# Kernel tuning notes

Measured on AMD Instinct MI355X. Metric: run time of the kernel, lower is better.

Reference implementation:

```python
import jax, jax.numpy as jnp
import numpy as np

N0, N1, N2 = 200000, 100000, 50000
E0, E1 = 1600000, 800000
D_IN, H, C, K = 256, 256, 7, 40  # in_feats, n_hidden, center_num, n_classes


def setup_inputs() -> dict:
    key = jax.random.key(0)
    ks = jax.random.split(key, 11)
    s = 0.05
    inputs = jax.random.normal(ks[0], (N0, D_IN), jnp.float32)
    edge_src0 = jax.random.randint(ks[1], (E0,), 0, N0, jnp.int32)
    edge_dst0 = jax.random.randint(ks[2], (E0,), 0, N1, jnp.int32)
    edge_src1 = jax.random.randint(ks[3], (E1,), 0, N1, jnp.int32)
    edge_dst1 = jax.random.randint(ks[4], (E1,), 0, N2, jnp.int32)
    W_self0 = jax.random.normal(ks[5], (H, D_IN), jnp.float32) * s
    W_neigh0 = jax.random.normal(ks[6], (H, D_IN), jnp.float32) * s
    b0 = jnp.zeros((H,), jnp.float32)
    W_self1 = jax.random.normal(ks[7], (H, H), jnp.float32) * s
    W_neigh1 = jax.random.normal(ks[8], (H, H), jnp.float32) * s
    b1 = jnp.zeros((H,), jnp.float32)
    W_prompt = jax.random.normal(ks[9], (C, 2 * H), jnp.float32) * s
    W_pp = jax.random.normal(ks[10], (C, K, 2 * H), jnp.float32) * s
    return dict(inputs=inputs, W_self0=W_self0, W_neigh0=W_neigh0, b0=b0,
                W_self1=W_self1, W_neigh1=W_neigh1, b1=b1,
                W_prompt=W_prompt, W_pp=W_pp,
                edge_src0=edge_src0, edge_dst0=edge_dst0,
                edge_src1=edge_src1, edge_dst1=edge_dst1)


def _sage_conv(h_src, h_dst, esrc, edst, n_dst, W_self, W_neigh, b):
    # DGL SAGEConv('mean'): fc_self(h_dst) + fc_neigh(mean_{u in N(v)} h_src[u]) + bias
    msg = h_src[esrc]                                            # [E, d]
    summ = jax.ops.segment_sum(msg, edst, num_segments=n_dst)    # [n_dst, d]
    deg = jax.ops.segment_sum(jnp.ones((esrc.shape[0],), msg.dtype), edst,
                              num_segments=n_dst)                # [n_dst]
    mean = summ / jnp.maximum(deg, 1.0)[:, None]
    return h_dst @ W_self.T + mean @ W_neigh.T + b


def _forward(inputs, W_self0, W_neigh0, b0, W_self1, W_neigh1, b1,
             W_prompt, W_pp, edge_src0, edge_dst0, edge_src1, edge_dst1):
    h = inputs  # dropout=0.0 (eval): identity
    # layer 0: N0 src -> N1 dst
    h_dst = h[:N1]
    h = _sage_conv(h, h_dst, edge_src0, edge_dst0, N1, W_self0, W_neigh0, b0)
    h = jax.nn.relu(h)
    # layer 1: N1 src -> N2 dst
    h_dst = h[:N2]
    h = _sage_conv(h, h_dst, edge_src1, edge_dst1, N2, W_self1, W_neigh1, b1)
    h = jax.nn.relu(h)
    neighbor = jax.nn.relu(h_dst)
    hcat = jnp.concatenate([h, neighbor], axis=1)                # [N2, 2H]
    scores = hcat @ W_prompt.T                                   # [N2, C]
    index = jnp.argmax(scores, axis=1)                           # [N2]
    # per-cluster expert Linear, top-1 dispatch/combine
    all_out = jnp.einsum('nd,ckd->nck', hcat, W_pp)              # [N2, C, K]
    out = jnp.take_along_axis(all_out, index[:, None, None], axis=1)[:, 0, :]
    return out


def reference(inputs, W_self0, W_neigh0, b0, W_self1, W_neigh1, b1,
              W_prompt, W_pp, edge_src0, edge_dst0, edge_src1, edge_dst1):
    return _forward(inputs, W_self0, W_neigh0, b0, W_self1, W_neigh1, b1,
                    W_prompt, W_pp, edge_src0, edge_dst0, edge_src1, edge_dst1)
```

## Files before the change

kernel.cpp:

```cpp
#include <hip/hip_runtime.h>
#include <stdint.h>

typedef unsigned short u16;
typedef unsigned int   u32;
typedef float f32x4  __attribute__((ext_vector_type(4)));
typedef _Float16 f16x4 __attribute__((ext_vector_type(4)));
typedef _Float16 f16x8 __attribute__((ext_vector_type(8)));

#define NN0 200000
#define NN1 100000
#define NN2 50000
#define EE0 1600000
#define EE1 800000
#define DD  256
#define CC  7
#define KK  40
#define NHEAD 288

#define LVL2_U16 4096
#define IMG_U16  8192

static __device__ __forceinline__ void split2(float x, _Float16& t0, _Float16& t1) {
    t0 = (_Float16)x;
    t1 = (_Float16)(x - (float)t0);
}

static __device__ __forceinline__ f16x8 pack8(const _Float16* h) {
    f16x8 v;
#pragma unroll
    for (int i = 0; i < 8; ++i) v[i] = h[i];
    return v;
}

static __device__ __forceinline__ void async16(const void* g, void* l) {
    __builtin_amdgcn_global_load_lds(
        (const __attribute__((address_space(1))) void*)g,
        (__attribute__((address_space(3))) void*)l, 16, 0, 0);
}

__global__ void hist_kernel(const int* __restrict__ dst, int* __restrict__ cnt, int n) {
    int i = blockIdx.x * blockDim.x + threadIdx.x;
    if (i < n) atomicAdd(&cnt[dst[i]], 1);
}

__global__ void scan_block_kernel(const int* __restrict__ in, int* __restrict__ out,
                                  int* __restrict__ partials, int n) {
    __shared__ int sd[256];
    int t = threadIdx.x;
    int base = blockIdx.x * 1024 + t * 4;
    int v0 = (base + 0 < n) ? in[base + 0] : 0;
    int v1 = (base + 1 < n) ? in[base + 1] : 0;
    int v2 = (base + 2 < n) ? in[base + 2] : 0;
    int v3 = (base + 3 < n) ? in[base + 3] : 0;
    int p0 = v0, p1 = p0 + v1, p2 = p1 + v2, p3 = p2 + v3;
    sd[t] = p3;
    __syncthreads();
    for (int off = 1; off < 256; off <<= 1) {
        int x = (t >= off) ? sd[t - off] : 0;
        __syncthreads();
        sd[t] += x;
        __syncthreads();
    }
    int excl = sd[t] - p3;
    if (base + 0 < n) out[base + 0] = excl + p0;
    if (base + 1 < n) out[base + 1] = excl + p1;
    if (base + 2 < n) out[base + 2] = excl + p2;
    if (base + 3 < n) out[base + 3] = excl + p3;
    if (t == 255) partials[blockIdx.x] = sd[255];
}

__global__ void scan_partials_kernel(int* __restrict__ partials, int nb) {
    __shared__ int sd[256];
    int t = threadIdx.x;
    int v = (t < nb) ? partials[t] : 0;
    sd[t] = v;
    __syncthreads();
    for (int off = 1; off < 256; off <<= 1) {
        int x = (t >= off) ? sd[t - off] : 0;
        __syncthreads();
        sd[t] += x;
        __syncthreads();
    }
    if (t < nb) partials[t] = sd[t];
}

__global__ void scan_add_kernel(int* __restrict__ out, const int* __restrict__ partials, int n) {
    int b = blockIdx.x;
    if (b == 0) return;
    int add = partials[b - 1];
    int base = b * 1024 + threadIdx.x * 4;
    if (base + 0 < n) out[base + 0] += add;
    if (base + 1 < n) out[base + 1] += add;
    if (base + 2 < n) out[base + 2] += add;
    if (base + 3 < n) out[base + 3] += add;
}

__global__ void fill_kernel(const int* __restrict__ esrc, const int* __restrict__ edst,
                            const int* __restrict__ rp, int* __restrict__ cur,
                            int* __restrict__ ss, int n) {
    int i = blockIdx.x * blockDim.x + threadIdx.x;
    if (i < n) {
        int d = edst[i];
        int p = rp[d] + atomicAdd(&cur[d], 1);
        ss[p] = esrc[i];
    }
}

__global__ void to_fp16(const float* __restrict__ in, _Float16* __restrict__ outp, long n) {
    long i = ((long)blockIdx.x * blockDim.x + threadIdx.x) * 8;
    if (i >= n) return;
    f32x4 a = *reinterpret_cast<const f32x4*>(in + i);
    f32x4 b = *reinterpret_cast<const f32x4*>(in + i + 4);
    f16x8 h;
    h[0] = (_Float16)a[0]; h[1] = (_Float16)a[1]; h[2] = (_Float16)a[2]; h[3] = (_Float16)a[3];
    h[4] = (_Float16)b[0]; h[5] = (_Float16)b[1]; h[6] = (_Float16)b[2]; h[7] = (_Float16)b[3];
    *reinterpret_cast<f16x8*>(outp + i) = h;
}

__global__ void gather_mean_fp16(const _Float16* __restrict__ Xh, const int* __restrict__ rp,
                                 const int* __restrict__ ss, float* __restrict__ mean, int ndst) {
    int wave = threadIdx.x >> 6, lane = threadIdx.x & 63;
    int d = blockIdx.x * 4 + wave;
    if (d >= ndst) return;
    int beg = rp[d], end = rp[d + 1];
    int lo4 = lane * 4;
    f32x4 a0 = (f32x4)(0.f), a1 = (f32x4)(0.f), a2 = (f32x4)(0.f), a3 = (f32x4)(0.f);
    int j = beg;
    for (; j + 8 <= end; j += 8) {
        int s0 = ss[j + 0], s1 = ss[j + 1], s2 = ss[j + 2], s3 = ss[j + 3];
        int s4 = ss[j + 4], s5 = ss[j + 5], s6 = ss[j + 6], s7 = ss[j + 7];
        f16x4 h0 = *reinterpret_cast<const f16x4*>(Xh + (size_t)s0 * DD + lo4);
        f16x4 h1 = *reinterpret_cast<const f16x4*>(Xh + (size_t)s1 * DD + lo4);
        f16x4 h2 = *reinterpret_cast<const f16x4*>(Xh + (size_t)s2 * DD + lo4);
        f16x4 h3 = *reinterpret_cast<const f16x4*>(Xh + (size_t)s3 * DD + lo4);
        f16x4 h4 = *reinterpret_cast<const f16x4*>(Xh + (size_t)s4 * DD + lo4);
        f16x4 h5 = *reinterpret_cast<const f16x4*>(Xh + (size_t)s5 * DD + lo4);
        f16x4 h6 = *reinterpret_cast<const f16x4*>(Xh + (size_t)s6 * DD + lo4);
        f16x4 h7 = *reinterpret_cast<const f16x4*>(Xh + (size_t)s7 * DD + lo4);
        a0 += __builtin_convertvector(h0, f32x4);
        a1 += __builtin_convertvector(h1, f32x4);
        a2 += __builtin_convertvector(h2, f32x4);
        a3 += __builtin_convertvector(h3, f32x4);
        a0 += __builtin_convertvector(h4, f32x4);
        a1 += __builtin_convertvector(h5, f32x4);
        a2 += __builtin_convertvector(h6, f32x4);
        a3 += __builtin_convertvector(h7, f32x4);
    }
    for (; j + 4 <= end; j += 4) {
        int s0 = ss[j + 0], s1 = ss[j + 1], s2 = ss[j + 2], s3 = ss[j + 3];
        f16x4 h0 = *reinterpret_cast<const f16x4*>(Xh + (size_t)s0 * DD + lo4);
        f16x4 h1 = *reinterpret_cast<const f16x4*>(Xh + (size_t)s1 * DD + lo4);
        f16x4 h2 = *reinterpret_cast<const f16x4*>(Xh + (size_t)s2 * DD + lo4);
        f16x4 h3 = *reinterpret_cast<const f16x4*>(Xh + (size_t)s3 * DD + lo4);
        a0 += __builtin_convertvector(h0, f32x4);
        a1 += __builtin_convertvector(h1, f32x4);
        a2 += __builtin_convertvector(h2, f32x4);
        a3 += __builtin_convertvector(h3, f32x4);
    }
    for (; j < end; ++j) {
        int s = ss[j];
        f16x4 h0 = *reinterpret_cast<const f16x4*>(Xh + (size_t)s * DD + lo4);
        a0 += __builtin_convertvector(h0, f32x4);
    }
    f32x4 s = (a0 + a1) + (a2 + a3);
    int dg = end - beg;
    float inv = 1.0f / (float)(dg > 0 ? dg : 1);
    s *= inv;
    *reinterpret_cast<f32x4*>(mean + (size_t)d * DD + lo4) = s;
}

__global__ void build_wimg(const float* __restrict__ Wa0, const float* __restrict__ Wb0,
                           const float* __restrict__ Wa1, const float* __restrict__ Wb1,
                           u16* __restrict__ img) {
    int blk = blockIdx.x;
    int layer = blk >> 5;
    int ntile = (blk >> 4) & 1;
    int chunk = blk & 15;
    const float* Wa = layer ? Wa1 : Wa0;
    const float* Wb = layer ? Wb1 : Wb0;
    int t = threadIdx.x;
    int row = t >> 1, half = t & 1;
    int n = ntile * 128 + row;
    int kg = chunk * 32 + half * 16;
    const float* W = (kg < 256) ? Wa : Wb;
    int kk = kg & 255;
    const float* src = W + (size_t)n * 256 + kk;
    float x[16];
#pragma unroll
    for (int j = 0; j < 16; j += 4) {
        float4 v = *reinterpret_cast<const float4*>(src + j);
        x[j] = v.x; x[j + 1] = v.y; x[j + 2] = v.z; x[j + 3] = v.w;
    }
    _Float16 h0[16], h1[16];
#pragma unroll
    for (int j = 0; j < 16; ++j) split2(x[j], h0[j], h1[j]);
    int rs = (row >> 1) & 3;
    int q0 = (half * 2 + 0) ^ rs;
    int q1 = (half * 2 + 1) ^ rs;
    u16* base = img + (size_t)blk * IMG_U16 + row * 32;
    *reinterpret_cast<f16x8*>(base + q0 * 8)            = pack8(h0);
    *reinterpret_cast<f16x8*>(base + q1 * 8)            = pack8(h0 + 8);
    *reinterpret_cast<f16x8*>(base + LVL2_U16 + q0 * 8) = pack8(h1);
    *reinterpret_cast<f16x8*>(base + LVL2_U16 + q1 * 8) = pack8(h1 + 8);
}

__global__ void build_wimg_head(const float* __restrict__ Wp, const float* __restrict__ Wpp,
                                u16* __restrict__ img) {
    int blk = blockIdx.x;
    int ntile = blk >> 4;
    int chunk = blk & 15;
    int t = threadIdx.x;
    int row = t >> 1, half = t & 1;
    int r = ntile * 128 + row;
    int kg = chunk * 32 + half * 16;
    float x[16];
    const float* src = nullptr;
    if (r < CC)            src = Wp  + (size_t)r * 512 + kg;
    else if (r < CC + CC * KK) src = Wpp + (size_t)(r - CC) * 512 + kg;
    if (src) {
#pragma unroll
        for (int j = 0; j < 16; j += 4) {
            float4 v = *reinterpret_cast<const float4*>(src + j);
            x[j] = v.x; x[j + 1] = v.y; x[j + 2] = v.z; x[j + 3] = v.w;
        }
    } else {
#pragma unroll
        for (int j = 0; j < 16; ++j) x[j] = 0.f;
    }
    _Float16 h0[16], h1[16];
#pragma unroll
    for (int j = 0; j < 16; ++j) split2(x[j], h0[j], h1[j]);
    int rs = (row >> 1) & 3;
    int q0 = (half * 2 + 0) ^ rs;
    int q1 = (half * 2 + 1) ^ rs;
    u16* base = img + (size_t)blk * IMG_U16 + row * 32;
    *reinterpret_cast<f16x8*>(base + q0 * 8)            = pack8(h0);
    *reinterpret_cast<f16x8*>(base + q1 * 8)            = pack8(h0 + 8);
    *reinterpret_cast<f16x8*>(base + LVL2_U16 + q0 * 8) = pack8(h1);
    *reinterpret_cast<f16x8*>(base + LVL2_U16 + q1 * 8) = pack8(h1 + 8);
}

__global__ __launch_bounds__(256, 3) void gemm_f16(const float* __restrict__ X0,
                                                   const float* __restrict__ X1,
                                                   const u16* __restrict__ imgL,
                                                   const float* __restrict__ bias,
                                                   float* __restrict__ out,
                                                   _Float16* __restrict__ outh,
                                                   int M, int ldo, int dorelu) {
    __shared__ __align__(16) u16 Asl[2 * LVL2_U16];
    __shared__ __align__(16) u16 Bsl[2 * LVL2_U16];
    int t = threadIdx.x;
    int wave = t >> 6, lane = t & 63;
    int m0 = blockIdx.x * 128;
    int ntile = blockIdx.y;
    int wy = wave >> 1, wx = wave & 1;

    f32x4 acc[4][4];
#pragma unroll
    for (int i = 0; i < 4; ++i)
#pragma unroll
        for (int j = 0; j < 4; ++j) acc[i][j] = (f32x4)(0.f);

    int arow_l = t >> 1;
    int akh = t & 1;
    int arow = m0 + arow_l; if (arow >= M) arow = M - 1;

    int fr = lane & 15;
    int q  = lane >> 4;
    int frm = wy * 64 + fr;
    int frn = wx * 64 + fr;

    const u16* imgT = imgL + (size_t)ntile * 16 * IMG_U16;

    for (int c = 0; c < 16; ++c) {
        const char* src = (const char*)(imgT + (size_t)c * IMG_U16);
#pragma unroll
        for (int i = 0; i < 4; ++i) {
            int seg = wave * 4 + i;
            async16(src + seg * 1024 + lane * 16, (char*)Bsl + seg * 1024 + lane * 16);
        }
        {
            const float* Xs = (c < 8) ? X0 : X1;
            int kc = (c & 7) * 32;
            const float* p = Xs + (size_t)arow * 256 + kc + akh * 16;
            float x[16];
#pragma unroll
            for (int j = 0; j < 16; j += 4) {
                float4 v = *reinterpret_cast<const float4*>(p + j);
                x[j] = v.x; x[j + 1] = v.y; x[j + 2] = v.z; x[j + 3] = v.w;
            }
            _Float16 h0[16], h1[16];
#pragma unroll
            for (int j = 0; j < 16; ++j) split2(x[j], h0[j], h1[j]);
            int rs = (arow_l >> 1) & 3;
            int q0 = (akh * 2 + 0) ^ rs;
            int q1 = (akh * 2 + 1) ^ rs;
            u16* d = Asl + arow_l * 32;
            *reinterpret_cast<f16x8*>(d + q0 * 8)            = pack8(h0);
            *reinterpret_cast<f16x8*>(d + q1 * 8)            = pack8(h0 + 8);
            *reinterpret_cast<f16x8*>(d + LVL2_U16 + q0 * 8) = pack8(h1);
            *reinterpret_cast<f16x8*>(d + LVL2_U16 + q1 * 8) = pack8(h1 + 8);
        }
        __syncthreads();
        f16x8 bf[4][2];
#pragma unroll
        for (int ns = 0; ns < 4; ++ns) {
            int r = frn + ns * 16;
            int off = r * 32 + ((q ^ ((r >> 1) & 3))) * 8;
            bf[ns][0] = *reinterpret_cast<const f16x8*>(Bsl + off);
            bf[ns][1] = *reinterpret_cast<const f16x8*>(Bsl + LVL2_U16 + off);
        }
#pragma unroll
        for (int ms = 0; ms < 4; ++ms) {
            int r = frm + ms * 16;
            int off = r * 32 + ((q ^ ((r >> 1) & 3))) * 8;
            f16x8 af0 = *reinterpret_cast<const f16x8*>(Asl + off);
            f16x8 af1 = *reinterpret_cast<const f16x8*>(Asl + LVL2_U16 + off);
#pragma unroll
            for (int ns = 0; ns < 4; ++ns) {
                f32x4 a = acc[ms][ns];
                a = __builtin_amdgcn_mfma_f32_16x16x32_f16(af0, bf[ns][0], a, 0, 0, 0);
                a = __builtin_amdgcn_mfma_f32_16x16x32_f16(af0, bf[ns][1], a, 0, 0, 0);
                a = __builtin_amdgcn_mfma_f32_16x16x32_f16(af1, bf[ns][0], a, 0, 0, 0);
                acc[ms][ns] = a;
            }
        }
        __syncthreads();
    }
#pragma unroll
    for (int ms = 0; ms < 4; ++ms) {
        int rbase = m0 + wy * 64 + ms * 16 + (lane >> 4) * 4;
#pragma unroll
        for (int ns = 0; ns < 4; ++ns) {
            int col = ntile * 128 + wx * 64 + ns * 16 + (lane & 15);
            if (col >= ldo) continue;
            float bcol = bias ? bias[col] : 0.f;
#pragma unroll
            for (int r = 0; r < 4; ++r) {
                int row = rbase + r;
                if (row < M) {
                    float v = acc[ms][ns][r] + bcol;
                    if (dorelu) v = fmaxf(v, 0.f);
                    out[(size_t)row * ldo + col] = v;
                    if (outh) outh[(size_t)row * DD + col] = (_Float16)v;
                }
            }
        }
    }
}

__global__ void select_kernel(const float* __restrict__ all, float* __restrict__ out) {
    int wave = threadIdx.x >> 6, lane = threadIdx.x & 63;
    int n = blockIdx.x * 4 + wave;
    if (n >= NN2) return;
    const float* row = all + (size_t)n * NHEAD;
    float best = row[0]; int bc = 0;
#pragma unroll
    for (int c = 1; c < CC; ++c) {
        float s = row[c];
        if (s > best) { best = s; bc = c; }
    }
    if (lane < KK) out[(size_t)n * KK + lane] = row[CC + bc * KK + lane];
}

extern "C" void kernel_launch(void* const* d_in, const int* in_sizes, int n_in,
                              void* d_out, int out_size, void* d_ws, size_t ws_size,
                              hipStream_t stream) {
    const float* inputs  = (const float*)d_in[0];
    const float* Wself0  = (const float*)d_in[1];
    const float* Wneigh0 = (const float*)d_in[2];
    const float* b0      = (const float*)d_in[3];
    const float* Wself1  = (const float*)d_in[4];
    const float* Wneigh1 = (const float*)d_in[5];
    const float* b1      = (const float*)d_in[6];
    const float* Wp      = (const float*)d_in[7];
    const float* Wpp     = (const float*)d_in[8];
    const int* es0 = (const int*)d_in[9];
    const int* ed0 = (const int*)d_in[10];
    const int* es1 = (const int*)d_in[11];
    const int* ed1 = (const int*)d_in[12];

    char* ws = (char*)d_ws;
    size_t off = 0;
    auto alloc = [&](size_t bytes) -> void* {
        void* p = (void*)(ws + off);
        off += (bytes + 255) & ~(size_t)255;
        return p;
    };
    int* cnt0 = (int*)alloc((size_t)NN1 * 4);
    int* cnt1 = (int*)alloc((size_t)NN2 * 4);
    int* cur0 = (int*)alloc((size_t)NN1 * 4);
    int* cur1 = (int*)alloc((size_t)NN2 * 4);
    int* rp0  = (int*)alloc((size_t)(NN1 + 1) * 4);
    int* rp1  = (int*)alloc((size_t)(NN2 + 1) * 4);
    int* part0 = (int*)alloc(1024);
    int* part1 = (int*)alloc(1024);
    size_t zero_bytes = off;
    int*   ss0   = (int*)alloc((size_t)EE0 * 4);
    int*   ss1   = (int*)alloc((size_t)EE1 * 4);
    u16*   wimg  = (u16*)alloc((size_t)(64 + 48) * IMG_U16 * 2);
    u16*   wimgH = wimg + (size_t)64 * IMG_U16;
    _Float16* xh = (_Float16*)alloc((size_t)NN0 * DD * 2);
    float*    h1 = (float*)xh;
    _Float16* h1h  = (_Float16*)alloc((size_t)NN1 * DD * 2);
    float* mean0 = (float*)alloc((size_t)NN1 * DD * 4);
    float* mean1 = mean0;
    float* h2    = mean0 + (size_t)NN2 * DD;
    float* allout = (float*)alloc((size_t)NN2 * NHEAD * 4);

    hipMemsetAsync(d_ws, 0, zero_bytes, stream);

    hist_kernel<<<(EE0 + 255) / 256, 256, 0, stream>>>(ed0, cnt0, EE0);
    hist_kernel<<<(EE1 + 255) / 256, 256, 0, stream>>>(ed1, cnt1, EE1);
    int nb0 = (NN1 + 1023) / 1024, nb1 = (NN2 + 1023) / 1024;
    scan_block_kernel<<<nb0, 256, 0, stream>>>(cnt0, rp0 + 1, part0, NN1);
    scan_partials_kernel<<<1, 256, 0, stream>>>(part0, nb0);
    scan_add_kernel<<<nb0, 256, 0, stream>>>(rp0 + 1, part0, NN1);
    scan_block_kernel<<<nb1, 256, 0, stream>>>(cnt1, rp1 + 1, part1, NN2);
    scan_partials_kernel<<<1, 256, 0, stream>>>(part1, nb1);
    scan_add_kernel<<<nb1, 256, 0, stream>>>(rp1 + 1, part1, NN2);
    fill_kernel<<<(EE0 + 255) / 256, 256, 0, stream>>>(es0, ed0, rp0, cur0, ss0, EE0);
    fill_kernel<<<(EE1 + 255) / 256, 256, 0, stream>>>(es1, ed1, rp1, cur1, ss1, EE1);

    build_wimg<<<64, 256, 0, stream>>>(Wself0, Wneigh0, Wself1, Wneigh1, wimg);
    build_wimg_head<<<48, 256, 0, stream>>>(Wp, Wpp, wimgH);

    long nx = (long)NN0 * DD;
    to_fp16<<<(int)(nx / 8 / 256), 256, 0, stream>>>(inputs, xh, nx);

    gather_mean_fp16<<<(NN1 + 3) / 4, 256, 0, stream>>>(xh, rp0, ss0, mean0, NN1);
    dim3 g0((NN1 + 127) / 128, 2);
    gemm_f16<<<g0, 256, 0, stream>>>(inputs, mean0, wimg, b0, h1, h1h, NN1, DD, 1);

    gather_mean_fp16<<<(NN2 + 3) / 4, 256, 0, stream>>>(h1h, rp1, ss1, mean1, NN2);
    dim3 g1((NN2 + 127) / 128, 2);
    gemm_f16<<<g1, 256, 0, stream>>>(h1, mean1, wimg + (size_t)32 * IMG_U16, b1, h2, nullptr, NN2, DD, 1);

    dim3 gh((NN2 + 127) / 128, 3);
    gemm_f16<<<gh, 256, 0, stream>>>(h2, h1, wimgH, nullptr, allout, nullptr, NN2, NHEAD, 0);
    select_kernel<<<(NN2 + 3) / 4, 256, 0, stream>>>(allout, (float*)d_out);
}
```

Measured before the change: 1.042 ms.

## Double-buffer B tiles and prefetch A into registers in gemm_f16

Restructures the gemm_f16 main loop into a software pipeline. The next chunk's B tile is fetched asynchronously into a second LDS buffer and the next A chunk is loaded into registers while the MFMAs for the current chunk run. A is written to LDS after a barrier, so global-load latency is meant to overlap with compute. The cost is more LDS (B doubled), which may reduce occupancy under launch_bounds(256,3), plus an extra barrier per iteration; the weight-image builders are also refactored to use shared helpers.

```diff
diff --git a/kernel.cpp b/kernel.cpp
--- a/kernel.cpp
+++ b/kernel.cpp
@@ -36,6 +36,24 @@
     __builtin_amdgcn_global_load_lds(
         (const __attribute__((address_space(1))) void*)g,
         (__attribute__((address_space(3))) void*)l, 16, 0, 0);
+}
+
+static __device__ __forceinline__ void loadA_f32(const float* p, float* xa) {
+#pragma unroll
+    for (int j = 0; j < 16; j += 4) {
+        float4 v = *reinterpret_cast<const float4*>(p + j);
+        xa[j] = v.x; xa[j + 1] = v.y; xa[j + 2] = v.z; xa[j + 3] = v.w;
+    }
+}
+
+static __device__ __forceinline__ void writeA_f32(const float* xa, u16* d, int q0, int q1) {
+    _Float16 h0[16], h1v[16];
+#pragma unroll
+    for (int j = 0; j < 16; ++j) split2(xa[j], h0[j], h1v[j]);
+    *reinterpret_cast<f16x8*>(d + q0 * 8)            = pack8(h0);
+    *reinterpret_cast<f16x8*>(d + q1 * 8)            = pack8(h0 + 8);
+    *reinterpret_cast<f16x8*>(d + LVL2_U16 + q0 * 8) = pack8(h1v);
+    *reinterpret_cast<f16x8*>(d + LVL2_U16 + q1 * 8) = pack8(h1v + 8);
 }
 
 __global__ void hist_kernel(const int* __restrict__ dst, int* __restrict__ cnt, int n) {
@@ -184,24 +202,12 @@
     int kg = chunk * 32 + half * 16;
     const float* W = (kg < 256) ? Wa : Wb;
     int kk = kg & 255;
-    const float* src = W + (size_t)n * 256 + kk;
     float x[16];
-#pragma unroll
-    for (int j = 0; j < 16; j += 4) {
-        float4 v = *reinterpret_cast<const float4*>(src + j);
-        x[j] = v.x; x[j + 1] = v.y; x[j + 2] = v.z; x[j + 3] = v.w;
-    }
-    _Float16 h0[16], h1[16];
-#pragma unroll
-    for (int j = 0; j < 16; ++j) split2(x[j], h0[j], h1[j]);
+    loadA_f32(W + (size_t)n * 256 + kk, x);
     int rs = (row >> 1) & 3;
     int q0 = (half * 2 + 0) ^ rs;
     int q1 = (half * 2 + 1) ^ rs;
-    u16* base = img + (size_t)blk * IMG_U16 + row * 32;
-    *reinterpret_cast<f16x8*>(base + q0 * 8)            = pack8(h0);
-    *reinterpret_cast<f16x8*>(base + q1 * 8)            = pack8(h0 + 8);
-    *reinterpret_cast<f16x8*>(base + LVL2_U16 + q0 * 8) = pack8(h1);
-    *reinterpret_cast<f16x8*>(base + LVL2_U16 + q1 * 8) = pack8(h1 + 8);
+    writeA_f32(x, img + (size_t)blk * IMG_U16 + row * 32, q0, q1);
 }
 
 __global__ void build_wimg_head(const float* __restrict__ Wp, const float* __restrict__ Wpp,
@@ -215,29 +221,17 @@
     int kg = chunk * 32 + half * 16;
     float x[16];
     const float* src = nullptr;
-    if (r < CC)            src = Wp  + (size_t)r * 512 + kg;
+    if (r < CC)                src = Wp  + (size_t)r * 512 + kg;
     else if (r < CC + CC * KK) src = Wpp + (size_t)(r - CC) * 512 + kg;
-    if (src) {
-#pragma unroll
-        for (int j = 0; j < 16; j += 4) {
-            float4 v = *reinterpret_cast<const float4*>(src + j);
-            x[j] = v.x; x[j + 1] = v.y; x[j + 2] = v.z; x[j + 3] = v.w;
-        }
-    } else {
+    if (src) loadA_f32(src, x);
+    else {
 #pragma unroll
         for (int j = 0; j < 16; ++j) x[j] = 0.f;
     }
-    _Float16 h0[16], h1[16];
-#pragma unroll
-    for (int j = 0; j < 16; ++j) split2(x[j], h0[j], h1[j]);
     int rs = (row >> 1) & 3;
     int q0 = (half * 2 + 0) ^ rs;
     int q1 = (half * 2 + 1) ^ rs;
-    u16* base = img + (size_t)blk * IMG_U16 + row * 32;
-    *reinterpret_cast<f16x8*>(base + q0 * 8)            = pack8(h0);
-    *reinterpret_cast<f16x8*>(base + q1 * 8)            = pack8(h0 + 8);
-    *reinterpret_cast<f16x8*>(base + LVL2_U16 + q0 * 8) = pack8(h1);
-    *reinterpret_cast<f16x8*>(base + LVL2_U16 + q1 * 8) = pack8(h1 + 8);
+    writeA_f32(x, img + (size_t)blk * IMG_U16 + row * 32, q0, q1);
 }
 
 __global__ __launch_bounds__(256, 3) void gemm_f16(const float* __restrict__ X0,
@@ -248,7 +242,7 @@
                                                    _Float16* __restrict__ outh,
                                                    int M, int ldo, int dorelu) {
     __shared__ __align__(16) u16 Asl[2 * LVL2_U16];
-    __shared__ __align__(16) u16 Bsl[2 * LVL2_U16];
+    __shared__ __align__(16) u16 Bsl[2][2 * LVL2_U16];
     int t = threadIdx.x;
     int wave = t >> 6, lane = t & 63;
     int m0 = blockIdx.x * 128;
@@ -264,6 +258,9 @@
     int arow_l = t >> 1;
     int akh = t & 1;
     int arow = m0 + arow_l; if (arow >= M) arow = M - 1;
+    int rsw = (arow_l >> 1) & 3;
+    int q0w = (akh * 2 + 0) ^ rsw;
+    int q1w = (akh * 2 + 1) ^ rsw;
 
     int fr = lane & 15;
     int q  = lane >> 4;
@@ -272,43 +269,44 @@
 
     const u16* imgT = imgL + (size_t)ntile * 16 * IMG_U16;
 
-    for (int c = 0; c < 16; ++c) {
-        const char* src = (const char*)(imgT + (size_t)c * IMG_U16);
+    float xa[16];
+
+    auto issueB = [&](int cc, int buf) {
+        const char* srcB = (const char*)(imgT + (size_t)cc * IMG_U16);
+        char* dstB = (char*)Bsl[buf];
 #pragma unroll
         for (int i = 0; i < 4; ++i) {
             int seg = wave * 4 + i;
-            async16(src + seg * 1024 + lane * 16, (char*)Bsl + seg * 1024 + lane * 16);
-        }
-        {
-            const float* Xs = (c < 8) ? X0 : X1;
-            int kc = (c & 7) * 32;
-            const float* p = Xs + (size_t)arow * 256 + kc + akh * 16;
-            float x[16];
-#pragma unroll
-            for (int j = 0; j < 16; j += 4) {
-                float4 v = *reinterpret_cast<const float4*>(p + j);
-                x[j] = v.x; x[j + 1] = v.y; x[j + 2] = v.z; x[j + 3] = v.w;
-            }
-            _Float16 h0[16], h1[16];
-#pragma unroll
-            for (int j = 0; j < 16; ++j) split2(x[j], h0[j], h1[j]);
-            int rs = (arow_l >> 1) & 3;
-            int q0 = (akh * 2 + 0) ^ rs;
-            int q1 = (akh * 2 + 1) ^ rs;
-            u16* d = Asl + arow_l * 32;
-            *reinterpret_cast<f16x8*>(d + q0 * 8)            = pack8(h0);
-            *reinterpret_cast<f16x8*>(d + q1 * 8)            = pack8(h0 + 8);
-            *reinterpret_cast<f16x8*>(d + LVL2_U16 + q0 * 8) = pack8(h1);
-            *reinterpret_cast<f16x8*>(d + LVL2_U16 + q1 * 8) = pack8(h1 + 8);
-        }
-        __syncthreads();
+            async16(srcB + seg * 1024 + lane * 16, dstB + seg * 1024 + lane * 16);
+        }
+    };
+    auto loadA = [&](int cc) {
+        const float* Xs = (cc < 8) ? X0 : X1;
+        loadA_f32(Xs + (size_t)arow * 256 + (cc & 7) * 32 + akh * 16, xa);
+    };
+    auto writeA = [&]() {
+        writeA_f32(xa, Asl + arow_l * 32, q0w, q1w);
+    };
+
+    issueB(0, 0);
+    loadA(0);
+    writeA();
+    __syncthreads();
+
+    for (int c = 0; c < 16; ++c) {
+        int nc = c + 1;
+        if (nc < 16) {
+            issueB(nc, nc & 1);
+            loadA(nc);
+        }
+        const u16* B = Bsl[c & 1];
         f16x8 bf[4][2];
 #pragma unroll
         for (int ns = 0; ns < 4; ++ns) {
             int r = frn + ns * 16;
             int off = r * 32 + ((q ^ ((r >> 1) & 3))) * 8;
-            bf[ns][0] = *reinterpret_cast<const f16x8*>(Bsl + off);
-            bf[ns][1] = *reinterpret_cast<const f16x8*>(Bsl + LVL2_U16 + off);
+            bf[ns][0] = *reinterpret_cast<const f16x8*>(B + off);
+            bf[ns][1] = *reinterpret_cast<const f16x8*>(B + LVL2_U16 + off);
         }
 #pragma unroll
         for (int ms = 0; ms < 4; ++ms) {
@@ -326,6 +324,10 @@
             }
         }
         __syncthreads();
+        if (nc < 16) {
+            writeA();
+            __syncthreads();
+        }
     }
 #pragma unroll
     for (int ms = 0; ms < 4; ++ms) {
```

Measured after the change: 1.084 ms. 1.04x slower.
